# Optimization experiments

Hardware: AMD Instinct MI355X
Metric: run time of the kernel (lower is better)

## Reference

```python
import jax, jax.numpy as jnp
import numpy as np

B, O, C, HID, H, W = 4, 8, 256, 128, 64, 64
STEPS = 2  # message passing steps


def _conv3x3(x, w, b):
    # x: [N,Cin,H,W], w: [Cout,Cin,3,3]
    y = jax.lax.conv_general_dilated(x, w, window_strides=(1, 1), padding='SAME',
                                     dimension_numbers=('NCHW', 'OIHW', 'NCHW'))
    return y + b[None, :, None, None]


def setup_inputs() -> dict:
    key = jax.random.key(0)
    ks = jax.random.split(key, 6)
    return {
        'batch_node_feats': jax.random.normal(ks[0], (B, C, H, W), jnp.float32),
        'batch_previous_masks': jax.random.uniform(ks[1], (B, O, H, W), jnp.float32),
        'batch_valid_indices': jnp.ones((B, O), jnp.bool_),
        'batch_previous_states': jnp.zeros((B, O), jnp.float32),  # unused (use_temporal_features=False)
        'enc_w': jax.random.normal(ks[2], (HID, C + 1, 3, 3), jnp.float32) * 0.02,
        'enc_b': jnp.zeros((HID,), jnp.float32),
        'gcn_w': jax.random.normal(ks[3], (HID, 2 * HID, 3, 3), jnp.float32) * 0.02,
        'gcn_b': jnp.zeros((HID,), jnp.float32),
        'ro_w': jax.random.normal(ks[4], (1, C + HID, 3, 3), jnp.float32) * 0.02,
        'ro_b': jnp.zeros((1,), jnp.float32),
    }


def reference(batch_node_feats, batch_previous_masks, batch_valid_indices,
              batch_previous_states, enc_w, enc_b, gcn_w, gcn_b, ro_w, ro_b):
    # All objects valid (batch_valid_indices all True) -> fully vectorized over B and O.
    feats = jnp.broadcast_to(batch_node_feats[:, None], (B, O, C, H, W))
    # Mask encoder: per-object state from frame feats + previous object mask.
    enc_in = jnp.concatenate([feats, batch_previous_masks[:, :, None]], axis=2)
    states = jax.nn.relu(_conv3x3(enc_in.reshape(B * O, C + 1, H, W), enc_w, enc_b))
    states = states.reshape(B, O, HID, H, W)
    # Fully-connected message passing: neighbors of i = all objects except i.
    for _ in range(STEPS):
        agg = states.sum(axis=1, keepdims=True) - states  # sum over others
        gcn_in = jnp.concatenate([states, agg], axis=2).reshape(B * O, 2 * HID, H, W)
        states = jax.nn.relu(_conv3x3(gcn_in, gcn_w, gcn_b)).reshape(B, O, HID, H, W)
    # Readout: per-object mask logits -> sigmoid.
    ro_in = jnp.concatenate([feats, states], axis=2).reshape(B * O, C + HID, H, W)
    out_masks = jax.nn.sigmoid(_conv3x3(ro_in, ro_w, ro_b)).reshape(B, O, H, W)
    return out_masks  # out_states is None when use_temporal_features=False
```

## Files before the change

kernel.cpp:

```cpp
#include <hip/hip_runtime.h>
#include <math.h>


typedef unsigned short ushort_t;
typedef _Float16 f16x8 __attribute__((ext_vector_type(8)));
typedef float f32x4 __attribute__((ext_vector_type(4)));

#define GLDS(gsrc, ldst)                                                      \
    __builtin_amdgcn_global_load_lds(                                         \
        (const __attribute__((address_space(1))) unsigned int*)(gsrc),        \
        (__attribute__((address_space(3))) unsigned int*)(ldst), 16, 0, 0)

__device__ __forceinline__ ushort_t f2h(float f) {
    _Float16 h = (_Float16)f;
    return *(ushort_t*)&h;
}
__device__ __forceinline__ float h2f(ushort_t u) {
    _Float16 h = *(_Float16*)&u;
    return (float)h;
}

__global__ __launch_bounds__(256) void prep_all(
    const float* __restrict__ feats, const float* __restrict__ enc_w,
    const float* __restrict__ gcn_w, const float* __restrict__ ro_w,
    ushort_t* __restrict__ featsT, ushort_t* __restrict__ WencF,
    ushort_t* __restrict__ WgcnS, ushort_t* __restrict__ WgcnD,
    ushort_t* __restrict__ WroQ, ushort_t* __restrict__ WroS)
{
    __shared__ float tile[64][65];
    int bid = blockIdx.x, t = threadIdx.x;
    if (bid < 1024) {
        int pt = bid & 63, ct = (bid >> 6) & 3, img = bid >> 8;
        int px_l = t & 63;
        const float* src = feats + ((size_t)img * 256 + ct * 64) * 4096 + pt * 64;
#pragma unroll
        for (int j = 0; j < 16; ++j) {
            int ci_l = (t >> 6) + j * 4;
            tile[px_l][ci_l] = src[(size_t)ci_l * 4096 + px_l];
        }
        __syncthreads();
        int px = t >> 2;
#pragma unroll
        for (int j = 0; j < 2; ++j) {
            int c8 = ((t & 3) + j * 4) * 8;
            uint4 v; ushort_t* pv = (ushort_t*)&v;
#pragma unroll
            for (int k = 0; k < 8; ++k) pv[k] = f2h(tile[px][c8 + k]);
            int cc = ct * 2 + (c8 >> 5);
            *(uint4*)(featsT + ((size_t)img * 8 + cc) * 131072 +
                      (size_t)(pt * 64 + px) * 32 + (c8 & 31)) = v;
        }
        return;
    }
    int i = (bid - 1024) * 256 + t;
    if (i < 294912) {
        int ci32 = i & 31, co = (i >> 5) & 127, tc = i >> 12;
        int tt = tc >> 3, cc = tc & 7, ci = cc * 32 + ci32;
        WencF[i] = f2h(enc_w[(co * 257 + ci) * 9 + tt]);
    } else if (i < 442368) {
        int j = i - 294912;
        int ci32 = j & 31, co = (j >> 5) & 127, tc = j >> 12;
        int tt = tc >> 2, cc = tc & 3, ci = cc * 32 + ci32;
        WgcnS[j] = f2h(gcn_w[(co * 256 + 128 + ci) * 9 + tt]);
    } else if (i < 589824) {
        int j = i - 442368;
        int ci32 = j & 31, co = (j >> 5) & 127, tc = j >> 12;
        int tt = tc >> 2, cc = tc & 3, ci = cc * 32 + ci32;
        WgcnD[j] = f2h(gcn_w[(co * 256 + ci) * 9 + tt] -
                       gcn_w[(co * 256 + 128 + ci) * 9 + tt]);
    } else if (i < 592128) {
        int j = i - 589824;
        int k = j & 7, r = j >> 3;
        int tt = r % 9, cq = r / 9, q = cq & 3, cc = cq >> 2;
        WroQ[j] = f2h(ro_w[(cc * 32 + q * 8 + k) * 9 + tt]);
    } else if (i < 593280) {
        int j = i - 592128;
        int k = j & 7, r = j >> 3;
        int tt = r % 9, cq = r / 9, q = cq & 3, cc = cq >> 2;
        WroS[j] = f2h(ro_w[(256 + cc * 32 + q * 8 + k) * 9 + tt]);
    }
}

template<int NCCBLK, bool FUSE, bool SUMIN>
__global__ __launch_bounds__(256, 3) void conv_k(
    const ushort_t* __restrict__ x, const ushort_t* __restrict__ W,
    ushort_t* __restrict__ out,
    const ushort_t* __restrict__ addp, const float* __restrict__ bias,
    int ncc_img)
{
    __shared__ ushort_t raw[25088];
    ushort_t* xs = raw;
    ushort_t* wlds = raw + 16896;
    ushort_t* eb16 = raw;

    const int rp = blockIdx.x, img = blockIdx.y, kz = blockIdx.z;
    const int row0 = rp * 2;
    const int cc0 = kz * NCCBLK;
    const int nchunk = 9 * NCCBLK;
    const int tid = threadIdx.x;
    const int w = tid >> 6, lane = tid & 63, lq = lane >> 4, lr = lane & 15;
    const int cg = w >> 1, pg = w & 1;

    const size_t objstride = (size_t)ncc_img * 131072;
    const ushort_t* xb = SUMIN ? x + (size_t)img * 8 * objstride
                               : x + (size_t)img * objstride;
    const int aoff0 = (cg * 64 + lr) * 32 + (lq ^ ((lr >> 1) & 3)) * 8;

    if (tid < 64) {
        int b = tid >> 5, r = (tid >> 3) & 3, c = (tid >> 2) & 1, s = tid & 3;
        *(uint4*)(xs + b * 8448 + r * 2112 + (c ? 65 : 0) * 32 + s * 8) =
            make_uint4(0, 0, 0, 0);
    }

    f32x4 acc[4][4];
#pragma unroll
    for (int a = 0; a < 4; ++a)
#pragma unroll
        for (int p = 0; p < 4; ++p) acc[a][p] = (f32x4){0.f, 0.f, 0.f, 0.f};

    const int gy = row0 - 1 + w;
    const bool row_ok = (unsigned)gy < 64u;
#define STAGE_ACT(cc_, buf_)                                                    \
    {                                                                           \
        ushort_t* dstrow = xs + (buf_) * 8448 + w * 2112;                       \
        if (row_ok) {                                                           \
            const ushort_t* src = xb + (size_t)(cc_) * 131072 + (size_t)gy * 2048; \
            if constexpr (SUMIN) {                                              \
                _Pragma("unroll")                                               \
                for (int u_ = 0; u_ < 4; ++u_) {                                \
                    f16x8 a_ = {0, 0, 0, 0, 0, 0, 0, 0};                        \
                    _Pragma("unroll")                                           \
                    for (int o_ = 0; o_ < 8; ++o_)                              \
                        a_ = a_ + *(const f16x8*)(src + (size_t)o_ * objstride + \
                                                  u_ * 512 + lane * 8);         \
                    int colp_ = 1 + u_ * 16 + (lane >> 2);                      \
                    int ssw_ = (lane & 3) ^ ((colp_ >> 1) & 3);                 \
                    *(f16x8*)(dstrow + colp_ * 32 + ssw_ * 8) = a_;             \
                }                                                               \
            } else {                                                            \
                _Pragma("unroll")                                               \
                for (int u_ = 0; u_ < 4; ++u_) {                                \
                    int colp_ = 1 + u_ * 16 + (lane >> 2);                      \
                    int ssw_ = (lane & 3) ^ ((colp_ >> 1) & 3);                 \
                    GLDS(src + (size_t)(colp_ - 1) * 32 + ssw_ * 8,             \
                         dstrow + 32 + u_ * 512);                               \
                }                                                               \
            }                                                                   \
        } else {                                                                \
            _Pragma("unroll")                                                   \
            for (int u_ = 0; u_ < 4; ++u_)                                      \
                *(uint4*)(dstrow + 32 + u_ * 512 + lane * 8) =                  \
                    make_uint4(0, 0, 0, 0);                                     \
        }                                                                       \
    }
#define STAGE_W(t_, cc_, buf_)                                                  \
    {                                                                           \
        const ushort_t* src = W + ((size_t)((t_) * ncc_img + (cc_)) * 4096);    \
        ushort_t* dst = wlds + (buf_) * 4096;                                   \
        _Pragma("unroll")                                                       \
        for (int j_ = 0; j_ < 2; ++j_) {                                        \
            int co_ = (w * 2 + j_) * 16 + (lane >> 2);                          \
            int ssw_ = (lane & 3) ^ ((co_ >> 1) & 3);                           \
            GLDS(src + co_ * 32 + ssw_ * 8, dst + (w * 2 + j_) * 512);          \
        }                                                                       \
    }

    STAGE_ACT(cc0, 0);
    STAGE_W(0, cc0, 0);

    int kc = 0;
#pragma unroll
    for (int ccl = 0; ccl < NCCBLK; ++ccl) {
        const int cc = cc0 + ccl;
        const int xbuf = ccl & 1;
#pragma unroll
        for (int t = 0; t < 9; ++t, ++kc) {
            __syncthreads();
            if (kc + 1 < nchunk) {
                if (t == 8) {
                    STAGE_W(0, cc + 1, (kc + 1) & 1);
                    STAGE_ACT(cc + 1, (ccl + 1) & 1);
                } else {
                    STAGE_W(t + 1, cc, (kc + 1) & 1);
                }
            }
            const int dy = t / 3, dx = t - 3 * dy;
            const ushort_t* wl = wlds + (kc & 1) * 4096 + aoff0;
            const int colb = dx + lr;
            const int swb = lq ^ ((colb >> 1) & 3);
            const ushort_t* xl = xs + xbuf * 8448 + (pg + dy) * 2112 +
                                 colb * 32 + swb * 8;
            f16x8 A0 = *(const f16x8*)(wl);
            f16x8 A1 = *(const f16x8*)(wl + 512);
            f16x8 A2 = *(const f16x8*)(wl + 1024);
            f16x8 A3 = *(const f16x8*)(wl + 1536);
#pragma unroll
            for (int p = 0; p < 4; ++p) {
                f16x8 Bf = *(const f16x8*)(xl + p * 512);
                acc[0][p] = __builtin_amdgcn_mfma_f32_16x16x32_f16(A0, Bf, acc[0][p], 0, 0, 0);
                acc[1][p] = __builtin_amdgcn_mfma_f32_16x16x32_f16(A1, Bf, acc[1][p], 0, 0, 0);
                acc[2][p] = __builtin_amdgcn_mfma_f32_16x16x32_f16(A2, Bf, acc[2][p], 0, 0, 0);
                acc[3][p] = __builtin_amdgcn_mfma_f32_16x16x32_f16(A3, Bf, acc[3][p], 0, 0, 0);
            }
        }
    }

    ushort_t* obase = out + (size_t)(kz * gridDim.y + img) * 524288;
    const int b4 = img >> 3;
#pragma unroll
    for (int r = 0; r < 2; ++r) {
        __syncthreads();
        if (pg == r) {
#pragma unroll
            for (int cf = 0; cf < 4; ++cf)
#pragma unroll
                for (int pf = 0; pf < 4; ++pf) {
                    int px = pf * 16 + lr;
                    int co_l = cg * 64 + cf * 16 + lq * 4;
                    ushort_t pk[4];
#pragma unroll
                    for (int j = 0; j < 4; ++j) pk[j] = f2h(acc[cf][pf][j]);
                    *(uint2*)(eb16 + px * 136 + co_l) = *(uint2*)pk;
                }
        }
        __syncthreads();
#pragma unroll
        for (int k2 = 0; k2 < 4; ++k2) {
            int i = tid + k2 * 256;
            int px = i >> 4, c16 = i & 15;
            int pxg = (row0 + r) * 64 + px;
            size_t coff = (size_t)(c16 >> 2) * 131072 + (size_t)pxg * 32 + (c16 & 3) * 8;
            uint4 v = *(uint4*)(eb16 + px * 136 + c16 * 8);
            if constexpr (FUSE) {
                const ushort_t* vp = (const ushort_t*)&v;
                float vv[8];
#pragma unroll
                for (int k = 0; k < 8; ++k) vv[k] = h2f(vp[k]) + bias[c16 * 8 + k];
#pragma unroll
                for (int p = 0; p < 4; ++p) {
                    uint4 av = *(const uint4*)(addp + (size_t)(p * 4 + b4) * 524288 + coff);
                    const ushort_t* ap = (const ushort_t*)&av;
#pragma unroll
                    for (int k = 0; k < 8; ++k) vv[k] += h2f(ap[k]);
                }
                uint4 sv; ushort_t* sp = (ushort_t*)&sv;
#pragma unroll
                for (int k = 0; k < 8; ++k) sp[k] = f2h(fmaxf(vv[k], 0.f));
                *(uint4*)(obase + coff) = sv;
            } else {
                *(uint4*)(obase + coff) = v;
            }
        }
    }
#undef STAGE_ACT
#undef STAGE_W
}

__global__ __launch_bounds__(256) void enc_obj_ro(
    const float* __restrict__ masks, const float* __restrict__ enc_w,
    const float* __restrict__ enc_b, const ushort_t* __restrict__ U1p,
    const ushort_t* __restrict__ featsT, const ushort_t* __restrict__ WroQ,
    ushort_t* __restrict__ S, ushort_t* __restrict__ USum,
    float* __restrict__ YR)
{
    int bid = blockIdx.x, tid = threadIdx.x;
    if (bid >= 1024) {
        int i = (bid - 1024) * 256 + tid;
        int cu = i & 31, px = (i >> 5) & 4095, b = i >> 17;
        int cc = cu >> 2, q = cu & 3;
        int y = px >> 6, xcol = px & 63;
        const ushort_t* wp = WroQ + (size_t)(cc * 4 + q) * 72;
        float wreg[9][8];
#pragma unroll
        for (int t = 0; t < 9; ++t) {
            uint4 wv = *(const uint4*)(wp + t * 8);
            const ushort_t* wq = (const ushort_t*)&wv;
#pragma unroll
            for (int k = 0; k < 8; ++k) wreg[t][k] = h2f(wq[k]);
        }
        const ushort_t* fb = featsT + (size_t)(b * 8 + cc) * 131072 + q * 8;
        float acc = 0.f;
#pragma unroll
        for (int dy = 0; dy < 3; ++dy) {
            int gy = y + dy - 1;
            if ((unsigned)gy >= 64u) continue;
#pragma unroll
            for (int dx = 0; dx < 3; ++dx) {
                int gx = xcol + dx - 1;
                if ((unsigned)gx >= 64u) continue;
                uint4 v = *(const uint4*)(fb + (size_t)(gy * 64 + gx) * 32);
                const ushort_t* vp = (const ushort_t*)&v;
#pragma unroll
                for (int k = 0; k < 8; ++k)
                    acc = fmaf(h2f(vp[k]), wreg[dy * 3 + dx][k], acc);
            }
        }
#pragma unroll
        for (int d = 16; d >= 1; d >>= 1) acc += __shfl_down(acc, d, 32);
        if (cu == 0) YR[b * 4096 + px] = acc;
        return;
    }
    int i = bid * 256 + tid;
    int s = i & 3, px = (i >> 2) & 4095, cc = (i >> 14) & 3, b = i >> 16;
    int co = cc * 32 + s * 8;
    int y = px >> 6, xx = px & 63;
    size_t coff = (size_t)cc * 131072 + (size_t)px * 32 + s * 8;
    float base[8];
#pragma unroll
    for (int k = 0; k < 8; ++k) base[k] = enc_b[co + k];
#pragma unroll
    for (int p = 0; p < 4; ++p) {
        uint4 v = *(const uint4*)(U1p + (size_t)(p * 4 + b) * 524288 + coff);
        const ushort_t* vp = (const ushort_t*)&v;
#pragma unroll
        for (int k = 0; k < 8; ++k) base[k] += h2f(vp[k]);
    }
    float wm[8][9];
#pragma unroll
    for (int k = 0; k < 8; ++k) {
        const float* wp = enc_w + (size_t)((co + k) * 257 + 256) * 9;
#pragma unroll
        for (int t = 0; t < 9; ++t) wm[k][t] = wp[t];
    }
    float sacc[8] = {0, 0, 0, 0, 0, 0, 0, 0};
#pragma unroll
    for (int o = 0; o < 8; ++o) {
        const float* m = masks + (size_t)(b * 8 + o) * 4096;
        float mt[9];
#pragma unroll
        for (int dy = 0; dy < 3; ++dy)
#pragma unroll
            for (int dx = 0; dx < 3; ++dx) {
                int gy_ = y + dy - 1, gx = xx + dx - 1;
                mt[dy * 3 + dx] =
                    ((unsigned)gy_ < 64u && (unsigned)gx < 64u) ? m[gy_ * 64 + gx] : 0.f;
            }
        uint4 sv; ushort_t* sp = (ushort_t*)&sv;
#pragma unroll
        for (int k = 0; k < 8; ++k) {
            float acc = base[k];
#pragma unroll
            for (int t = 0; t < 9; ++t) acc = fmaf(mt[t], wm[k][t], acc);
            acc = fmaxf(acc, 0.f);
            sacc[k] += acc;
            sp[k] = f2h(acc);
        }
        *(uint4*)(S + (size_t)(b * 8 + o) * 524288 + coff) = sv;
    }
    uint4 sv; ushort_t* sp = (ushort_t*)&sv;
#pragma unroll
    for (int k = 0; k < 8; ++k) sp[k] = f2h(sacc[k]);
    *(uint4*)(USum + (size_t)b * 524288 + coff) = sv;
}

__global__ __launch_bounds__(256) void ro_obj(
    const ushort_t* __restrict__ S, const ushort_t* __restrict__ WroS,
    const float* __restrict__ ro_b, const float* __restrict__ YR,
    float* __restrict__ out)
{
    int i = blockIdx.x * 256 + threadIdx.x;
    int cu = i & 15, px = (i >> 4) & 4095, n = i >> 16;
    int b = n >> 3;
    int cc = cu >> 2, q = cu & 3;
    int y = px >> 6, xcol = px & 63;
    const ushort_t* wp = WroS + (size_t)(cc * 4 + q) * 72;
    float wreg[9][8];
#pragma unroll
    for (int t = 0; t < 9; ++t) {
        uint4 wv = *(const uint4*)(wp + t * 8);
        const ushort_t* wq = (const ushort_t*)&wv;
#pragma unroll
        for (int k = 0; k < 8; ++k) wreg[t][k] = h2f(wq[k]);
    }
    const ushort_t* sb = S + ((size_t)n * 4 + cc) * 131072 + q * 8;
    float acc = 0.f;
#pragma unroll
    for (int dy = 0; dy < 3; ++dy) {
        int gy = y + dy - 1;
        if ((unsigned)gy >= 64u) continue;
#pragma unroll
        for (int dx = 0; dx < 3; ++dx) {
            int gx = xcol + dx - 1;
            if ((unsigned)gx >= 64u) continue;
            uint4 v = *(const uint4*)(sb + (size_t)(gy * 64 + gx) * 32);
            const ushort_t* vp = (const ushort_t*)&v;
#pragma unroll
            for (int k = 0; k < 8; ++k)
                acc = fmaf(h2f(vp[k]), wreg[dy * 3 + dx][k], acc);
        }
    }
#pragma unroll
    for (int d = 8; d >= 1; d >>= 1) acc += __shfl_down(acc, d, 16);
    if (cu == 0) {
        float v = acc + YR[b * 4096 + px] + ro_b[0];
        out[n * 4096 + px] = 1.f / (1.f + __expf(-v));
    }
}

extern "C" void kernel_launch(void* const* d_in, const int* in_sizes, int n_in,
                              void* d_out, int out_size, void* d_ws, size_t ws_size,
                              hipStream_t stream)
{
    const float* feats = (const float*)d_in[0];
    const float* masks = (const float*)d_in[1];
    const float* enc_w = (const float*)d_in[4];
    const float* enc_b = (const float*)d_in[5];
    const float* gcn_w = (const float*)d_in[6];
    const float* gcn_b = (const float*)d_in[7];
    const float* ro_w  = (const float*)d_in[8];
    const float* ro_b  = (const float*)d_in[9];
    float* out = (float*)d_out;

    ushort_t* WencF  = (ushort_t*)d_ws;
    ushort_t* WgcnS  = WencF + 294912;
    ushort_t* WgcnD  = WgcnS + 147456;
    ushort_t* WroQ   = WgcnD + 147456;
    ushort_t* WroS   = WroQ + 2304;
    ushort_t* featsT = WroS + 1152;
    ushort_t* Sa     = featsT + 4194304;
    ushort_t* Sb     = Sa + 16777216;
    ushort_t* USum   = Sb + 16777216;
    ushort_t* U1p16  = USum + 2097152;
    ushort_t* U2p16  = U1p16 + 8388608;
    float*    YR     = (float*)(U2p16 + 8388608);

    dim3 blk(256);

    prep_all<<<3344, blk, 0, stream>>>(feats, enc_w, gcn_w, ro_w,
                                       featsT, WencF, WgcnS, WgcnD, WroQ, WroS);

    conv_k<2, false, false><<<dim3(32, 4, 4), blk, 0, stream>>>(
        featsT, WencF, U1p16, nullptr, nullptr, 8);
    enc_obj_ro<<<3072, blk, 0, stream>>>(masks, enc_w, enc_b, U1p16,
                                         featsT, WroQ, Sa, USum, YR);

    conv_k<1, false, false><<<dim3(32, 4, 4), blk, 0, stream>>>(
        USum, WgcnS, U2p16, nullptr, nullptr, 4);
    conv_k<4, true, false><<<dim3(32, 32, 1), blk, 0, stream>>>(
        Sa, WgcnD, Sb, U2p16, gcn_b, 4);

    conv_k<1, false, true><<<dim3(32, 4, 4), blk, 0, stream>>>(
        Sb, WgcnS, U2p16, nullptr, nullptr, 4);
    conv_k<4, true, false><<<dim3(32, 32, 1), blk, 0, stream>>>(
        Sb, WgcnD, Sa, U2p16, gcn_b, 4);

    ro_obj<<<8192, blk, 0, stream>>>(Sa, WroS, ro_b, YR, out);
}
```

Measured before the change: 266.6 us.

## Rework conv pipeline with triple-buffered weights, single act buffer and manual waitcnts

The conv kernel now keeps a single activation buffer without padding columns and masks the image edges in registers instead. Weights are triple-buffered and prefetched two chunks ahead, synchronised with explicit vmcnt/lgkmcnt waits and raw barriers in place of __syncthreads. The smaller LDS footprint lets the launch bound rise to 4 blocks per CU, and MFMA issue is raised with s_setprio. The trade-off is that activation loads at each channel-chunk boundary are no longer prefetched, so they are exposed behind an extra barrier.

```diff
diff --git a/kernel.cpp b/kernel.cpp
--- a/kernel.cpp
+++ b/kernel.cpp
@@ -10,6 +10,10 @@
     __builtin_amdgcn_global_load_lds(                                         \
         (const __attribute__((address_space(1))) unsigned int*)(gsrc),        \
         (__attribute__((address_space(3))) unsigned int*)(ldst), 16, 0, 0)
+
+#define WAITVM0() asm volatile("s_waitcnt vmcnt(0)" ::: "memory")
+#define WAITVM2() asm volatile("s_waitcnt vmcnt(2)" ::: "memory")
+#define WAITLGKM0() asm volatile("s_waitcnt lgkmcnt(0)" ::: "memory")
 
 __device__ __forceinline__ ushort_t f2h(float f) {
     _Float16 h = (_Float16)f;
@@ -82,15 +86,15 @@
 }
 
 template<int NCCBLK, bool FUSE, bool SUMIN>
-__global__ __launch_bounds__(256, 3) void conv_k(
+__global__ __launch_bounds__(256, 4) void conv_k(
     const ushort_t* __restrict__ x, const ushort_t* __restrict__ W,
     ushort_t* __restrict__ out,
     const ushort_t* __restrict__ addp, const float* __restrict__ bias,
     int ncc_img)
 {
-    __shared__ ushort_t raw[25088];
+    __shared__ ushort_t raw[20480];
     ushort_t* xs = raw;
-    ushort_t* wlds = raw + 16896;
+    ushort_t* wlds = raw + 8192;
     ushort_t* eb16 = raw;
 
     const int rp = blockIdx.x, img = blockIdx.y, kz = blockIdx.z;
@@ -106,12 +110,6 @@
                                : x + (size_t)img * objstride;
     const int aoff0 = (cg * 64 + lr) * 32 + (lq ^ ((lr >> 1) & 3)) * 8;
 
-    if (tid < 64) {
-        int b = tid >> 5, r = (tid >> 3) & 3, c = (tid >> 2) & 1, s = tid & 3;
-        *(uint4*)(xs + b * 8448 + r * 2112 + (c ? 65 : 0) * 32 + s * 8) =
-            make_uint4(0, 0, 0, 0);
-    }
-
     f32x4 acc[4][4];
 #pragma unroll
     for (int a = 0; a < 4; ++a)
@@ -120,9 +118,9 @@
 
     const int gy = row0 - 1 + w;
     const bool row_ok = (unsigned)gy < 64u;
-#define STAGE_ACT(cc_, buf_)                                                    \
+#define STAGE_ACT(cc_)                                                          \
     {                                                                           \
-        ushort_t* dstrow = xs + (buf_) * 8448 + w * 2112;                       \
+        ushort_t* dstrow = xs + w * 2048;                                       \
         if (row_ok) {                                                           \
             const ushort_t* src = xb + (size_t)(cc_) * 131072 + (size_t)gy * 2048; \
             if constexpr (SUMIN) {                                              \
@@ -133,23 +131,23 @@
                     for (int o_ = 0; o_ < 8; ++o_)                              \
                         a_ = a_ + *(const f16x8*)(src + (size_t)o_ * objstride + \
                                                   u_ * 512 + lane * 8);         \
-                    int colp_ = 1 + u_ * 16 + (lane >> 2);                      \
+                    int colp_ = u_ * 16 + (lane >> 2);                          \
                     int ssw_ = (lane & 3) ^ ((colp_ >> 1) & 3);                 \
                     *(f16x8*)(dstrow + colp_ * 32 + ssw_ * 8) = a_;             \
                 }                                                               \
             } else {                                                            \
                 _Pragma("unroll")                                               \
                 for (int u_ = 0; u_ < 4; ++u_) {                                \
-                    int colp_ = 1 + u_ * 16 + (lane >> 2);                      \
+                    int colp_ = u_ * 16 + (lane >> 2);                          \
                     int ssw_ = (lane & 3) ^ ((colp_ >> 1) & 3);                 \
-                    GLDS(src + (size_t)(colp_ - 1) * 32 + ssw_ * 8,             \
-                         dstrow + 32 + u_ * 512);                               \
+                    GLDS(src + (size_t)colp_ * 32 + ssw_ * 8,                   \
+                         dstrow + u_ * 512);                                    \
                 }                                                               \
             }                                                                   \
         } else {                                                                \
             _Pragma("unroll")                                                   \
             for (int u_ = 0; u_ < 4; ++u_)                                      \
-                *(uint4*)(dstrow + 32 + u_ * 512 + lane * 8) =                  \
+                *(uint4*)(dstrow + u_ * 512 + lane * 8) =                       \
                     make_uint4(0, 0, 0, 0);                                     \
         }                                                                       \
     }
@@ -165,43 +163,62 @@
         }                                                                       \
     }
 
-    STAGE_ACT(cc0, 0);
+    STAGE_ACT(cc0);
     STAGE_W(0, cc0, 0);
-
-    int kc = 0;
+    if (nchunk > 1) STAGE_W(1, cc0, 1);
+    WAITLGKM0();
+
 #pragma unroll
     for (int ccl = 0; ccl < NCCBLK; ++ccl) {
         const int cc = cc0 + ccl;
-        const int xbuf = ccl & 1;
-#pragma unroll
-        for (int t = 0; t < 9; ++t, ++kc) {
-            __syncthreads();
-            if (kc + 1 < nchunk) {
-                if (t == 8) {
-                    STAGE_W(0, cc + 1, (kc + 1) & 1);
-                    STAGE_ACT(cc + 1, (ccl + 1) & 1);
-                } else {
-                    STAGE_W(t + 1, cc, (kc + 1) & 1);
-                }
-            }
+#pragma unroll
+        for (int t = 0; t < 9; ++t) {
+            const int kc = ccl * 9 + t;
+            if (kc == nchunk - 1) { WAITVM0(); }
+            else { WAITVM2(); }
+            __builtin_amdgcn_s_barrier();
+
+            if (t == 0 && ccl > 0) {
+                STAGE_ACT(cc);
+                if (kc + 2 < nchunk)
+                    STAGE_W((kc + 2) % 9, cc0 + (kc + 2) / 9, (kc + 2) % 3);
+                WAITVM2();
+                WAITLGKM0();
+                __builtin_amdgcn_s_barrier();
+            } else if (kc + 2 < nchunk) {
+                STAGE_W((kc + 2) % 9, cc0 + (kc + 2) / 9, (kc + 2) % 3);
+            }
+
             const int dy = t / 3, dx = t - 3 * dy;
-            const ushort_t* wl = wlds + (kc & 1) * 4096 + aoff0;
-            const int colb = dx + lr;
-            const int swb = lq ^ ((colb >> 1) & 3);
-            const ushort_t* xl = xs + xbuf * 8448 + (pg + dy) * 2112 +
-                                 colb * 32 + swb * 8;
+            const ushort_t* wl = wlds + (kc % 3) * 4096 + aoff0;
             f16x8 A0 = *(const f16x8*)(wl);
             f16x8 A1 = *(const f16x8*)(wl + 512);
             f16x8 A2 = *(const f16x8*)(wl + 1024);
             f16x8 A3 = *(const f16x8*)(wl + 1536);
+            const ushort_t* xrow = xs + (pg + dy) * 2048;
+            f16x8 Bf[4];
 #pragma unroll
             for (int p = 0; p < 4; ++p) {
-                f16x8 Bf = *(const f16x8*)(xl + p * 512);
-                acc[0][p] = __builtin_amdgcn_mfma_f32_16x16x32_f16(A0, Bf, acc[0][p], 0, 0, 0);
-                acc[1][p] = __builtin_amdgcn_mfma_f32_16x16x32_f16(A1, Bf, acc[1][p], 0, 0, 0);
-                acc[2][p] = __builtin_amdgcn_mfma_f32_16x16x32_f16(A2, Bf, acc[2][p], 0, 0, 0);
-                acc[3][p] = __builtin_amdgcn_mfma_f32_16x16x32_f16(A3, Bf, acc[3][p], 0, 0, 0);
-            }
+                int c = dx - 1 + lr + 16 * p;
+                int c2 = c;
+                bool edge = false;
+                if (dx == 0 && p == 0) { edge = (c < 0); c2 = c < 0 ? 0 : c; }
+                if (dx == 2 && p == 3) { edge = (c > 63); c2 = c > 63 ? 63 : c; }
+                f16x8 v = *(const f16x8*)(xrow + c2 * 32 +
+                                          ((lq ^ ((c2 >> 1) & 3))) * 8);
+                if (edge) v = (f16x8){0, 0, 0, 0, 0, 0, 0, 0};
+                Bf[p] = v;
+            }
+
+            __builtin_amdgcn_s_setprio(1);
+#pragma unroll
+            for (int p = 0; p < 4; ++p) {
+                acc[0][p] = __builtin_amdgcn_mfma_f32_16x16x32_f16(A0, Bf[p], acc[0][p], 0, 0, 0);
+                acc[1][p] = __builtin_amdgcn_mfma_f32_16x16x32_f16(A1, Bf[p], acc[1][p], 0, 0, 0);
+                acc[2][p] = __builtin_amdgcn_mfma_f32_16x16x32_f16(A2, Bf[p], acc[2][p], 0, 0, 0);
+                acc[3][p] = __builtin_amdgcn_mfma_f32_16x16x32_f16(A3, Bf[p], acc[3][p], 0, 0, 0);
+            }
+            __builtin_amdgcn_s_setprio(0);
         }
     }
 
```

Result: slower. 291.8 us (+9.4%).
